# Kernel tuning notes

Measured on AMD Instinct MI355X. Metric: run time of the kernel, lower is better.

The kernel has to match this reference:

```python
import jax, jax.numpy as jnp
import numpy as np

C = 768
HEADS = 12
NF = 8      # num_frames
SL = 196    # seq_len (patches per frame)
B = 2
N = 1 + NF * SL
HID = 4 * C


def _ln(x, g, b, eps=1e-5):
    mu = jnp.mean(x, axis=-1, keepdims=True)
    var = jnp.mean((x - mu) ** 2, axis=-1, keepdims=True)
    return (x - mu) * jax.lax.rsqrt(var + eps) * g + b


def setup_inputs() -> dict:
    key = jax.random.key(0)
    ks = jax.random.split(key, 16)
    s = 0.02
    return {
        "x": jax.random.normal(ks[0], (B, N, C), jnp.float32),
        "g1": jnp.ones((C,), jnp.float32),
        "b1": jnp.zeros((C,), jnp.float32),
        "Wqkv": jax.random.normal(ks[1], (C, 3 * C), jnp.float32) * s,
        "Wq": jax.random.normal(ks[2], (C, C), jnp.float32) * s,
        "Wkv": jax.random.normal(ks[3], (C, 2 * C), jnp.float32) * s,
        "Wp": jax.random.normal(ks[4], (C, C), jnp.float32) * s,
        "bp": jnp.zeros((C,), jnp.float32),
        "g2": jnp.ones((C,), jnp.float32),
        "b2": jnp.zeros((C,), jnp.float32),
        "W1": jax.random.normal(ks[5], (C, HID), jnp.float32) * s,
        "bf1": jnp.zeros((HID,), jnp.float32),
        "W2": jax.random.normal(ks[6], (HID, C), jnp.float32) * s,
        "bf2": jnp.zeros((C,), jnp.float32),
        "seq_len": SL,
        "num_frames": NF,
    }


def _traj_attn(xn, Wqkv, Wq, Wkv, Wp, bp, P, F):
    Bb, Nn, Cc = xn.shape
    h = HEADS
    d = Cc // h
    scale = d ** -0.5
    S = F * P  # non-cls tokens

    qkv = xn @ Wqkv                                   # (B,N,3C)
    q, k, v = jnp.split(qkv, 3, axis=-1)

    def heads(t):  # (B,N,C) -> (B*h, N, d)
        return t.reshape(Bb, Nn, h, d).transpose(0, 2, 1, 3).reshape(Bb * h, Nn, d)

    q, k, v = heads(q), heads(k), heads(v)
    cls_q, q_ = q[:, :1], q[:, 1:]
    k_ = k[:, 1:]
    v_ = v[:, 1:]

    # cls token attends to all tokens
    sim = jnp.einsum('bid,bjd->bij', cls_q * scale, k)
    cls_out = jnp.einsum('bij,bjd->bid', jax.nn.softmax(sim, axis=-1), v)
    cls_out = cls_out.reshape(Bb, h, 1, d).transpose(0, 2, 1, 3).reshape(Bb, 1, Cc)

    # stage 1: space-only softmax per frame
    qk = jnp.einsum('bqd,bkd->bqk', q_, k_).reshape(Bb * h, S, F, P)
    space_attn = jax.nn.softmax(scale * qk, axis=-1)          # (Bh,S,F,P)
    v_r = v_.reshape(Bb * h, F, P, d)
    x1 = jnp.einsum('bqfn,bfnd->bqfd', space_attn, v_r)       # (Bh,S,F,d)
    x1 = x1.reshape(Bb, h, S, F, d).transpose(0, 2, 3, 1, 4).reshape(Bb, S, F, Cc)

    # diagonal across (query-frame, key-frame)
    xg = x1.reshape(Bb, F, P, F, Cc)
    diag = jnp.diagonal(xg, axis1=1, axis2=3)                 # (B,P,C,F)
    x_diag = diag.transpose(0, 3, 1, 2).reshape(Bb, S, Cc)    # b (f n) d

    # stage 2: frame-wise attention
    q2 = (x_diag @ Wq).reshape(Bb, S, h, d).transpose(0, 2, 1, 3) * scale  # bhsd
    kv2 = x1 @ Wkv
    k2, v2 = jnp.split(kv2, 2, axis=-1)
    k2 = k2.reshape(Bb, S, F, h, d).transpose(0, 3, 1, 2, 4)  # bhsfd
    attn2 = jax.nn.softmax(jnp.einsum('bhsd,bhsfd->bhsf', q2, k2), axis=-1)
    xo = x1.reshape(Bb, S, F, h, d).transpose(0, 3, 1, 2, 4)  # use_original_code=True
    out = jnp.einsum('bhsf,bhsfd->bhsd', attn2, xo)
    out = out.transpose(0, 2, 1, 3).reshape(Bb, S, Cc)

    out = jnp.concatenate([cls_out, out], axis=1) @ Wp + bp
    return out


def reference(x, g1, b1, Wqkv, Wq, Wkv, Wp, bp, g2, b2, W1, bf1, W2, bf2, seq_len, num_frames):
    x = x + _traj_attn(_ln(x, g1, b1), Wqkv, Wq, Wkv, Wp, bp, seq_len, num_frames)
    h = _ln(x, g2, b2)
    h = jax.nn.gelu(h @ W1 + bf1, approximate=False) @ W2 + bf2
    return x + h
```

## Files before the change

kernel.cpp:

```cpp
#include <hip/hip_runtime.h>
#include <hip/hip_bf16.h>
#include <math.h>

#define C     768
#define HEADS 12
#define HD    64
#define NF    8
#define SL    196
#define BB    2
#define NN    1569
#define SS    1568
#define HID   3072
#define CLS_CH 256
#define CLS_NC 7
#define QSCALE 0.18033688011112042f

typedef __attribute__((ext_vector_type(8))) short short8;
typedef __attribute__((ext_vector_type(4))) float f32x4;
typedef unsigned short u16;
typedef unsigned int u32;

__device__ inline float fast_exp2(float x) { return __builtin_amdgcn_exp2f(x); }

__device__ inline u16 f2b(float f) {
    __hip_bfloat16 h = __float2bfloat16(f);
    return *reinterpret_cast<u16*>(&h);
}
__device__ inline float b2f(u16 u) {
    union { unsigned u; float f; } v; v.u = ((unsigned)u) << 16;
    return v.f;
}

__device__ inline void gload_lds16(const void* g, void* l) {
    __builtin_amdgcn_global_load_lds(
        (const __attribute__((address_space(1))) void*)g,
        (__attribute__((address_space(3))) void*)l, 16, 0, 0);
}

__global__ void ln_kernel(const float* __restrict__ x, const float* __restrict__ g,
                          const float* __restrict__ b, u16* __restrict__ out, int rows) {
    int row = blockIdx.x;
    if (row >= rows) return;
    const float* xr = x + (size_t)row * C;
    int tid = threadIdx.x;
    float v[3];
    float sum = 0.f, sumsq = 0.f;
#pragma unroll
    for (int i = 0; i < 3; i++) {
        v[i] = xr[tid + 256 * i];
        sum += v[i]; sumsq += v[i] * v[i];
    }
    __shared__ float s1[4], s2[4];
    for (int off = 32; off; off >>= 1) {
        sum   += __shfl_xor(sum, off);
        sumsq += __shfl_xor(sumsq, off);
    }
    int wave = tid >> 6, lane = tid & 63;
    if (lane == 0) { s1[wave] = sum; s2[wave] = sumsq; }
    __syncthreads();
    sum   = s1[0] + s1[1] + s1[2] + s1[3];
    sumsq = s2[0] + s2[1] + s2[2] + s2[3];
    float mu  = sum / C;
    float var = sumsq / C - mu * mu;
    float rstd = rsqrtf(fmaxf(var, 0.f) + 1e-5f);
    u16* outr = out + (size_t)row * C;
#pragma unroll
    for (int i = 0; i < 3; i++) {
        int c = tid + 256 * i;
        outr[c] = f2b((v[i] - mu) * rstd * g[c] + b[c]);
    }
}

__global__ void wtrans_all_kernel(
    const float* __restrict__ Wqkv, const float* __restrict__ Wq,
    const float* __restrict__ Wkv,  const float* __restrict__ Wp,
    const float* __restrict__ W1,   const float* __restrict__ W2,
    u16* Tqkv, u16* Tq, u16* Tkv, u16* Tp, u16* T1, u16* T2) {
    __shared__ float tile[64][65];
    int bid = blockIdx.x;
    const float* W; u16* Wt; int K, ldb, gx;
    if (bid < 432)       { W = Wqkv; Wt = Tqkv; K = 768;  ldb = 2304; gx = 36; }
    else if (bid < 576)  { W = Wq;   Wt = Tq;   K = 768;  ldb = 768;  gx = 12; bid -= 432; }
    else if (bid < 720)  { W = Wkv;  Wt = Tkv;  K = 768;  ldb = 1536; gx = 12; bid -= 576; }
    else if (bid < 864)  { W = Wp;   Wt = Tp;   K = 768;  ldb = 768;  gx = 12; bid -= 720; }
    else if (bid < 1440) { W = W1;   Wt = T1;   K = 768;  ldb = 3072; gx = 48; bid -= 864; }
    else                 { W = W2;   Wt = T2;   K = 3072; ldb = 768;  gx = 12; bid -= 1440; }
    int nb = (bid % gx) * 64, kb = (bid / gx) * 64;
    int tx = threadIdx.x & 63, ty = threadIdx.x >> 6;
#pragma unroll
    for (int i = 0; i < 64; i += 4)
        tile[ty + i][tx] = W[(size_t)(kb + ty + i) * ldb + nb + tx];
    __syncthreads();
#pragma unroll
    for (int i = 0; i < 64; i += 4)
        Wt[(size_t)(nb + ty + i) * K + kb + tx] = f2b(tile[tx][ty + i]);
}

template<int MODE, int BM, int BN, int WAVES>
__global__ __launch_bounds__(WAVES * 64) void gemm_bf16(
    const u16* __restrict__ A, const u16* __restrict__ Bt,
    const float* __restrict__ bias, const float* resid, void* Cout,
    int M, int N, int K, int lda, int ldb, int gx) {
    constexpr int WCOLS = WAVES / 2;
    constexpr int WBN   = BN / WCOLS;
    constexpr int MT    = BM / 32;
    constexpr int NT    = WBN / 16;
    constexpr int ACH   = BM * 4;
    constexpr int TCH   = (BM + BN) * 4;
    constexpr int HALF  = (BM + BN) * 64;
    __shared__ char smem[2 * HALF];
    int tid = threadIdx.x, lane = tid & 63, wave = tid >> 6;
    int wr = wave / WCOLS, wc = wave % WCOLS;
    int r16 = lane & 15, kg = lane >> 4;

    int nwg = gridDim.x, orig = blockIdx.x;
    int qq = nwg >> 3, rr = nwg & 7, xcd = orig & 7, lid = orig >> 3;
    int wg = (xcd < rr ? xcd * (qq + 1) : rr * (qq + 1) + (xcd - rr) * qq) + lid;
    int bx = wg % gx, by = wg / gx;
    if constexpr (MODE == 4) {
        int mt_ = (M + BM - 1) / BM;
        int chunk = by / mt_; by -= chunk * mt_;
        A    += (size_t)chunk * K;
        Bt   += (size_t)chunk * K;
        Cout  = (void*)((float*)Cout + (size_t)chunk * ((size_t)M * N));
    }
    int row0 = by * BM, col0 = bx * BN;

    f32x4 acc[MT][NT];
#pragma unroll
    for (int mt = 0; mt < MT; mt++)
#pragma unroll
        for (int nt = 0; nt < NT; nt++) acc[mt][nt] = (f32x4){0.f, 0.f, 0.f, 0.f};

    auto stage = [&](char* dstbase, int ks) {
        int k0 = ks << 5;
#pragma unroll
        for (int it = 0; it < TCH / (WAVES * 64); it++) {
            int c = it * (WAVES * 64) + tid;
            const u16* src;
            if (c < ACH) {
                int ml = c >> 2, s = c & 3;
                int kgs = s ^ ((ml >> 1) & 3);
                int gm = row0 + ml; if (gm >= M) gm = M - 1;
                src = A + (size_t)gm * lda + k0 + kgs * 8;
            } else {
                int cc = c - ACH;
                int nl = cc >> 2, s = cc & 3;
                int kgs = s ^ ((nl >> 1) & 3);
                src = Bt + (size_t)(col0 + nl) * ldb + k0 + kgs * 8;
            }
            gload_lds16(src, dstbase + it * (WAVES * 1024) + wave * 1024);
        }
    };

    int nsteps = K >> 5;
    stage(smem, 0);
    __syncthreads();
    for (int ks = 0; ks < nsteps; ks++) {
        char* curb = smem + (ks & 1) * HALF;
        if (ks + 1 < nsteps) stage(smem + ((ks + 1) & 1) * HALF, ks + 1);
        short8 af[MT], bfr[NT];
#pragma unroll
        for (int mt = 0; mt < MT; mt++) {
            int ml = wr * (BM / 2) + mt * 16 + r16;
            af[mt] = *(const short8*)(curb + ml * 64 + ((kg ^ ((ml >> 1) & 3)) << 4));
        }
#pragma unroll
        for (int nt = 0; nt < NT; nt++) {
            int nl = wc * WBN + nt * 16 + r16;
            bfr[nt] = *(const short8*)(curb + BM * 64 + nl * 64 + ((kg ^ ((nl >> 1) & 3)) << 4));
        }
        __builtin_amdgcn_s_setprio(1);
#pragma unroll
        for (int mt = 0; mt < MT; mt++)
#pragma unroll
            for (int nt = 0; nt < NT; nt++)
                acc[mt][nt] = __builtin_amdgcn_mfma_f32_16x16x32_bf16(af[mt], bfr[nt], acc[mt][nt], 0, 0, 0);
        __builtin_amdgcn_s_setprio(0);
        __syncthreads();
    }
#pragma unroll
    for (int mt = 0; mt < MT; mt++) {
#pragma unroll
        for (int r2 = 0; r2 < 4; r2++) {
            int gm = row0 + wr * (BM / 2) + mt * 16 + kg * 4 + r2;
            if (gm >= M) continue;
#pragma unroll
            for (int nt = 0; nt < NT; nt++) {
                int gn = col0 + wc * WBN + nt * 16 + r16;
                float v = acc[mt][nt][r2];
                if constexpr (MODE == 1) {
                    v += bias[gn];
                    v = 0.5f * v * (1.f + erff(v * 0.70710678118f));
                }
                if constexpr (MODE == 2) {
                    v += bias[gn] + resid[(size_t)gm * N + gn];
                    ((float*)Cout)[(size_t)gm * N + gn] = v;
                } else if constexpr (MODE == 4) {
                    ((float*)Cout)[(size_t)gm * N + gn] = v;
                } else {
                    if constexpr (MODE == 3) { if (gn < 768) v *= QSCALE; }
                    ((u16*)Cout)[(size_t)gm * N + gn] = f2b(v);
                }
            }
        }
    }
}

__global__ void fc2_merge_kernel(const float* __restrict__ p,
                                 const float* __restrict__ bias, float* __restrict__ out) {
    int i = blockIdx.x * 256 + threadIdx.x;
    int total = BB * NN * (C / 4);
    if (i >= total) return;
    int c4 = i % (C / 4);
    size_t stride = (size_t)BB * NN * (C / 4);
    float4 bb = ((const float4*)bias)[c4];
    float4 a0 = ((const float4*)p)[i];
    float4 a1 = ((const float4*)p)[i + stride];
    float4 o  = ((float4*)out)[i];
    o.x += a0.x + a1.x + bb.x;
    o.y += a0.y + a1.y + bb.y;
    o.z += a0.z + a1.z + bb.z;
    o.w += a0.w + a1.w + bb.w;
    ((float4*)out)[i] = o;
}

__global__ void cls_partial_kernel(const u16* __restrict__ qkv, float* __restrict__ part) {
    int c = blockIdx.x, bh = blockIdx.y;
    int b = bh / HEADS, hh = bh % HEADS;
    int tid = threadIdx.x;
    int wave = tid >> 6, lane = tid & 63;
    __shared__ float s_q[HD];
    __shared__ float s_sc[CLS_CH];
    __shared__ float sm[4], ss[4];
    __shared__ float sacc[4][HD];
    if (tid < HD) s_q[tid] = b2f(qkv[(size_t)(b * NN) * 2304 + hh * HD + tid]);
    __syncthreads();

    int j0 = c * CLS_CH;
    int j = j0 + tid;
    float sc = -1e30f;
    if (j < NN) {
        const short8* kp = (const short8*)(qkv + ((size_t)(b * NN) + j) * 2304 + C + hh * HD);
        float acc = 0.f;
#pragma unroll
        for (int u = 0; u < 8; u++) {
            short8 kv = kp[u];
#pragma unroll
            for (int e = 0; e < 8; e++) acc += s_q[u * 8 + e] * b2f((u16)kv[e]);
        }
        sc = acc;
    }
    float m = sc;
    for (int off = 32; off; off >>= 1) m = fmaxf(m, __shfl_xor(m, off));
    if (lane == 0) sm[wave] = m;
    __syncthreads();
    m = fmaxf(fmaxf(sm[0], sm[1]), fmaxf(sm[2], sm[3]));
    float e = (j < NN) ? fast_exp2(sc - m) : 0.f;
    s_sc[tid] = e;
    float su = e;
    for (int off = 32; off; off >>= 1) su += __shfl_xor(su, off);
    if (lane == 0) ss[wave] = su;
    __syncthreads();
    float ssum = ss[0] + ss[1] + ss[2] + ss[3];

    int jj = tid >> 6, d = tid & 63;
    int jmax = NN - j0; if (jmax > CLS_CH) jmax = CLS_CH;
    const u16* vcol = qkv + ((size_t)(b * NN) + j0) * 2304 + 2 * C + hh * HD + d;
    float acc = 0.f;
    for (int t = jj; t < jmax; t += 4)
        acc += s_sc[t] * b2f(vcol[(size_t)t * 2304]);
    sacc[jj][d] = acc;
    __syncthreads();
    if (tid < HD) {
        float pv = sacc[0][tid] + sacc[1][tid] + sacc[2][tid] + sacc[3][tid];
        float* pp = part + ((size_t)bh * CLS_NC + c) * 66;
        pp[2 + tid] = pv;
        if (tid == 0) { pp[0] = m; pp[1] = ssum; }
    }
}

__global__ void cls_reduce_kernel(const float* __restrict__ part, u16* __restrict__ y) {
    int bh = blockIdx.x;
    int b = bh / HEADS, hh = bh % HEADS;
    int d = threadIdx.x;
    float gm = -1e30f;
#pragma unroll
    for (int c = 0; c < CLS_NC; c++)
        gm = fmaxf(gm, part[((size_t)bh * CLS_NC + c) * 66]);
    float tot = 0.f, pv = 0.f;
#pragma unroll
    for (int c = 0; c < CLS_NC; c++) {
        const float* pp = part + ((size_t)bh * CLS_NC + c) * 66;
        float w = fast_exp2(pp[0] - gm);
        tot += pp[1] * w;
        pv  += pp[2 + d] * w;
    }
    y[(size_t)(b * NN) * C + hh * HD + d] = f2b(pv / tot);
}

__global__ void repack_kv_kernel(const u16* __restrict__ qkv,
                                 u16* __restrict__ Kb, u16* __restrict__ Vt) {
    const int NK = 24 * NF * 208 * 8;
    const int NV = 24 * NF * 64 * 28;
    int t = blockIdx.x * 256 + threadIdx.x;
    if (t < NK) {
        int d8 = t & 7;
        int rest = t >> 3;
        int n = rest % 208;
        rest /= 208;
        int f = rest % NF;
        int bh = rest / NF;
        int b = bh / HEADS, h = bh % HEADS;
        short8 v = {0, 0, 0, 0, 0, 0, 0, 0};
        if (n < SL)
            v = *(const short8*)(qkv + ((size_t)(b * NN) + 1 + f * SL + n) * 2304 + C + h * HD + d8 * 8);
        *(short8*)(Kb + (((size_t)bh * NF + f) * 208 + n) * 64 + d8 * 8) = v;
    } else {
        int u = t - NK;
        if (u >= NV) return;
        int n8 = u % 28;
        int rest = u / 28;
        int d = rest % 64;
        rest /= 64;
        int f = rest % NF;
        int bh = rest / NF;
        int b = bh / HEADS, h = bh % HEADS;
        int n0 = n8 * 8;
        const u16* src = qkv + ((size_t)(b * NN) + 1 + f * SL) * 2304 + 2 * C + h * HD + d;
        short8 v;
#pragma unroll
        for (int jj = 0; jj < 8; jj++) {
            int n = n0 + jj;
            v[jj] = (n < SL) ? (short)src[(size_t)n * 2304] : (short)0;
        }
        *(short8*)(Vt + (((size_t)bh * NF + f) * 64 + d) * 224 + n0) = v;
    }
}

__global__ void space_attn_mfma(
    const u16* __restrict__ qkv, const u16* __restrict__ Kb,
    const u16* __restrict__ Vt, u16* __restrict__ x1, u16* __restrict__ xd) {
    __shared__ u16 smem[13312];
    int tid = threadIdx.x;
    int lane = tid & 63, wave = tid >> 6;
    int r16 = lane & 15, kg = lane >> 4;

    int n = blockIdx.x;
    int xcd = n & 7;
    int slot = n >> 3;
    int j = slot % 13;
    int gw = slot / 13;
    int bh = xcd * 3 + gw % 3;
    int f = gw / 3;
    int b = bh / HEADS, h = bh % HEADS;

    int sA = j * 8 + wave * 2, sB = sA + 1;
    bool actA = sA < 98, actB = sB < 98;
    int q0A = (actA ? sA : 97) * 16;
    int q0B = (actB ? sB : 97) * 16;

    const u16* qrowA = qkv + ((size_t)(b * NN) + 1 + q0A + r16) * 2304 + h * HD + kg * 8;
    const u16* qrowB = qkv + ((size_t)(b * NN) + 1 + q0B + r16) * 2304 + h * HD + kg * 8;
    short8 aqA0 = *(const short8*)(qrowA);
    short8 aqA1 = *(const short8*)(qrowA + 32);
    short8 aqB0 = *(const short8*)(qrowB);
    short8 aqB1 = *(const short8*)(qrowB + 32);

    const char* kb_g = (const char*)(Kb + ((size_t)bh * NF + f) * 208 * 64);
    for (int w = wave; w < 26; w += 4) {
        int p = w * 1024 + lane * 16;
        int row = p >> 7;
        int src = (p & ~127) | ((p & 127) ^ ((row & 7) << 4));
        gload_lds16(kb_g + src, (char*)smem + p);
    }
    __syncthreads();

    const char* ksm = (const char*)smem;
    int swz = (r16 & 7) << 4;
    bool tailz = (kg >= 1);
    const u16* vbase = Vt + ((size_t)bh * NF + f) * 64 * 224;

    f32x4 acc[13];
    u32 w0A[13], w1A[13], w0B[13], w1B[13];

#pragma unroll
    for (int t = 0; t < 13; t++) acc[t] = (f32x4){0.f, 0.f, 0.f, 0.f};
    __builtin_amdgcn_s_setprio(1);
#pragma unroll
    for (int t = 0; t < 13; t++) {
        const char* krow = ksm + (t * 16 + r16) * 128;
        short8 bk0 = *(const short8*)(krow + ((kg * 16) ^ swz));
        short8 bk1 = *(const short8*)(krow + ((64 + kg * 16) ^ swz));
        acc[t] = __builtin_amdgcn_mfma_f32_16x16x32_bf16(bk0, aqA0, acc[t], 0, 0, 0);
        acc[t] = __builtin_amdgcn_mfma_f32_16x16x32_bf16(bk1, aqA1, acc[t], 0, 0, 0);
    }
    __builtin_amdgcn_s_setprio(0);
    short8 vf[2][4];
#pragma unroll
    for (int dt = 0; dt < 4; dt++)
        vf[0][dt] = *(const short8*)(vbase + (dt * 16 + r16) * 224 + kg * 8);
    {
        float ssum = 0.f;
#pragma unroll
        for (int t = 0; t < 13; t++)
#pragma unroll
            for (int r = 0; r < 4; r++) {
                float p = (t == 12 && tailz) ? 0.f : fast_exp2(acc[t][r]);
                acc[t][r] = p;
                ssum += p;
            }
        ssum += __shfl_xor(ssum, 16);
        ssum += __shfl_xor(ssum, 32);
        float inv = 1.f / ssum;
#pragma unroll
        for (int t = 0; t < 13; t++) {
            w0A[t] = (u32)f2b(acc[t][0] * inv) | ((u32)f2b(acc[t][1] * inv) << 16);
            w1A[t] = (u32)f2b(acc[t][2] * inv) | ((u32)f2b(acc[t][3] * inv) << 16);
        }
    }

#pragma unroll
    for (int t = 0; t < 13; t++) acc[t] = (f32x4){0.f, 0.f, 0.f, 0.f};
    __builtin_amdgcn_s_setprio(1);
#pragma unroll
    for (int t = 0; t < 13; t++) {
        const char* krow = ksm + (t * 16 + r16) * 128;
        short8 bk0 = *(const short8*)(krow + ((kg * 16) ^ swz));
        short8 bk1 = *(const short8*)(krow + ((64 + kg * 16) ^ swz));
        acc[t] = __builtin_amdgcn_mfma_f32_16x16x32_bf16(bk0, aqB0, acc[t], 0, 0, 0);
        acc[t] = __builtin_amdgcn_mfma_f32_16x16x32_bf16(bk1, aqB1, acc[t], 0, 0, 0);
    }
    __builtin_amdgcn_s_setprio(0);
    {
        float ssum = 0.f;
#pragma unroll
        for (int t = 0; t < 13; t++)
#pragma unroll
            for (int r = 0; r < 4; r++) {
                float p = (t == 12 && tailz) ? 0.f : fast_exp2(acc[t][r]);
                acc[t][r] = p;
                ssum += p;
            }
        ssum += __shfl_xor(ssum, 16);
        ssum += __shfl_xor(ssum, 32);
        float inv = 1.f / ssum;
#pragma unroll
        for (int t = 0; t < 13; t++) {
            w0B[t] = (u32)f2b(acc[t][0] * inv) | ((u32)f2b(acc[t][1] * inv) << 16);
            w1B[t] = (u32)f2b(acc[t][2] * inv) | ((u32)f2b(acc[t][3] * inv) << 16);
        }
    }

    int src0 = r16 + ((kg & 1) << 5);
    int src1 = src0 + 16;
    bool thi = (kg >= 2);
    f32x4 oA[4], oB[4];
#pragma unroll
    for (int dt = 0; dt < 4; dt++) { oA[dt] = (f32x4){0.f, 0.f, 0.f, 0.f}; oB[dt] = (f32x4){0.f, 0.f, 0.f, 0.f}; }
    __builtin_amdgcn_s_setprio(1);
#pragma unroll
    for (int kc = 0; kc < 7; kc++) {
        if (kc < 6) {
#pragma unroll
            for (int dt = 0; dt < 4; dt++)
                vf[(kc + 1) & 1][dt] = *(const short8*)(vbase + (dt * 16 + r16) * 224 + (kc + 1) * 32 + kg * 8);
        }
        u32 a0, a1, b0, b1;
        if (kc == 6) {
            a0 = thi ? 0u : w0A[12]; a1 = thi ? 0u : w1A[12];
            b0 = thi ? 0u : w0B[12]; b1 = thi ? 0u : w1B[12];
        } else {
            a0 = thi ? w0A[2 * kc + 1] : w0A[2 * kc];
            a1 = thi ? w1A[2 * kc + 1] : w1A[2 * kc];
            b0 = thi ? w0B[2 * kc + 1] : w0B[2 * kc];
            b1 = thi ? w1B[2 * kc + 1] : w1B[2 * kc];
        }
        union { u32 u[4]; short8 s8; } pA, pB;
        pA.u[0] = (u32)__shfl((int)a0, src0);
        pA.u[1] = (u32)__shfl((int)a1, src0);
        pA.u[2] = (u32)__shfl((int)a0, src1);
        pA.u[3] = (u32)__shfl((int)a1, src1);
        pB.u[0] = (u32)__shfl((int)b0, src0);
        pB.u[1] = (u32)__shfl((int)b1, src0);
        pB.u[2] = (u32)__shfl((int)b0, src1);
        pB.u[3] = (u32)__shfl((int)b1, src1);
#pragma unroll
        for (int dt = 0; dt < 4; dt++) {
            oA[dt] = __builtin_amdgcn_mfma_f32_16x16x32_bf16(pA.s8, vf[kc & 1][dt], oA[dt], 0, 0, 0);
            oB[dt] = __builtin_amdgcn_mfma_f32_16x16x32_bf16(pB.s8, vf[kc & 1][dt], oB[dt], 0, 0, 0);
        }
    }
    __builtin_amdgcn_s_setprio(0);

    __syncthreads();
    u16* ebA = smem + wave * 2304;
    u16* ebB = ebA + 1152;
    int fbase = f * SL;
#pragma unroll
    for (int dt = 0; dt < 4; dt++)
#pragma unroll
        for (int r = 0; r < 4; r++) {
            ebA[(kg * 4 + r) * 72 + dt * 16 + r16] = f2b(oA[dt][r]);
            ebB[(kg * 4 + r) * 72 + dt * 16 + r16] = f2b(oB[dt][r]);
        }
    if (actA) {
        u16* x1row = x1 + (((size_t)(b * SS + q0A)) * NF + f) * C + h * HD;
        u16* xdrow = xd + ((size_t)(b * SS + q0A)) * C + h * HD;
#pragma unroll
        for (int it = 0; it < 2; it++) {
            int c = it * 64 + lane;
            int qr = c >> 3, c8 = c & 7;
            short8 v8 = *(const short8*)(&ebA[qr * 72 + c8 * 8]);
            *(short8*)(x1row + (size_t)qr * (NF * C) + c8 * 8) = v8;
            if ((unsigned)(q0A + qr - fbase) < (unsigned)SL)
                *(short8*)(xdrow + (size_t)qr * C + c8 * 8) = v8;
        }
    }
    if (actB) {
        u16* x1row = x1 + (((size_t)(b * SS + q0B)) * NF + f) * C + h * HD;
        u16* xdrow = xd + ((size_t)(b * SS + q0B)) * C + h * HD;
#pragma unroll
        for (int it = 0; it < 2; it++) {
            int c = it * 64 + lane;
            int qr = c >> 3, c8 = c & 7;
            short8 v8 = *(const short8*)(&ebB[qr * 72 + c8 * 8]);
            *(short8*)(x1row + (size_t)qr * (NF * C) + c8 * 8) = v8;
            if ((unsigned)(q0B + qr - fbase) < (unsigned)SL)
                *(short8*)(xdrow + (size_t)qr * C + c8 * 8) = v8;
        }
    }
}

__global__ void attn2_kernel(const u16* __restrict__ q2, const u16* __restrict__ k2,
                             const u16* __restrict__ x1, u16* __restrict__ y) {
    int item = blockIdx.x * 4 + (threadIdx.x >> 6);
    if (item >= BB * HEADS * SS) return;
    int lane = threadIdx.x & 63;
    int s = item % SS;
    int bh = item / SS;
    int b = bh / HEADS, hh = bh % HEADS;
    size_t rowbs = (size_t)(b * SS + s);
    float qv = b2f(q2[rowbs * C + hh * HD + lane]) * QSCALE;
    float lg[NF];
#pragma unroll
    for (int f = 0; f < NF; f++) {
        float p = qv * b2f(k2[(rowbs * NF + f) * C + hh * HD + lane]);
        for (int off = 32; off; off >>= 1) p += __shfl_xor(p, off);
        lg[f] = p;
    }
    float m = lg[0];
#pragma unroll
    for (int f = 1; f < NF; f++) m = fmaxf(m, lg[f]);
    float sum = 0.f;
#pragma unroll
    for (int f = 0; f < NF; f++) { lg[f] = fast_exp2(lg[f] - m); sum += lg[f]; }
    float inv = 1.f / sum;
    float acc = 0.f;
#pragma unroll
    for (int f = 0; f < NF; f++) acc += lg[f] * b2f(x1[(rowbs * NF + f) * C + hh * HD + lane]);
    y[((size_t)(b * NN) + 1 + s) * C + hh * HD + lane] = f2b(acc * inv);
}

extern "C" void kernel_launch(void* const* d_in, const int* in_sizes, int n_in,
                              void* d_out, int out_size, void* d_ws, size_t ws_size,
                              hipStream_t stream) {
    const float* x    = (const float*)d_in[0];
    const float* g1   = (const float*)d_in[1];
    const float* b1   = (const float*)d_in[2];
    const float* Wqkv = (const float*)d_in[3];
    const float* Wq   = (const float*)d_in[4];
    const float* Wkv  = (const float*)d_in[5];
    const float* Wp   = (const float*)d_in[6];
    const float* bp   = (const float*)d_in[7];
    const float* g2   = (const float*)d_in[8];
    const float* b2_  = (const float*)d_in[9];
    const float* W1   = (const float*)d_in[10];
    const float* bf1  = (const float*)d_in[11];
    const float* W2   = (const float*)d_in[12];
    const float* bf2  = (const float*)d_in[13];
    float* out = (float*)d_out;

    u16* us     = (u16*)d_ws;
    u16* xn_b   = us;
    u16* qkv_b  = xn_b   + 2409984;
    u16* Wt_qkv = qkv_b  + 7229952;
    u16* Wt_q   = Wt_qkv + 1769472;
    u16* Wt_kv  = Wt_q   + 589824;
    u16* Wt_p   = Wt_kv  + 589824;
    u16* W1t    = Wt_p   + 589824;
    u16* W2t    = W1t    + 2359296;
    u16* Kb     = W2t    + 2359296;
    u16* Vt     = Kb     + 2555904;
    u16* x1b    = Vt     + 2752512;
    u16* xdb    = x1b    + 19267584;
    u16* q2b    = xdb    + 2408448;
    u16* k2b    = q2b    + 2408448;
    u16* y_b    = k2b    + 19267584;
    u16* a1b    = y_b    + 2409984;
    float* cls_ws   = (float*)(a1b + 9639936);
    float* fc2_part = cls_ws + 24 * 7 * 66;

    const int M1 = BB * NN;
    const int M2 = BB * SS;
    const int M3 = BB * SS * NF;

    wtrans_all_kernel<<<2016, 256, 0, stream>>>(Wqkv, Wq, Wkv, Wp, W1, W2,
                                                Wt_qkv, Wt_q, Wt_kv, Wt_p, W1t, W2t);
    ln_kernel<<<M1, 256, 0, stream>>>(x, g1, b1, xn_b, M1);
    gemm_bf16<3, 128, 128, 8><<<18 * 25, 512, 0, stream>>>(
        xn_b, Wt_qkv, nullptr, nullptr, qkv_b, M1, 2304, 768, 768, 768, 18);
    repack_kv_kernel<<<(24 * NF * 208 * 8 + 24 * NF * 64 * 28 + 255) / 256, 256, 0, stream>>>(
        qkv_b, Kb, Vt);
    cls_partial_kernel<<<dim3(CLS_NC, BB * HEADS), 256, 0, stream>>>(qkv_b, cls_ws);
    cls_reduce_kernel<<<BB * HEADS, 64, 0, stream>>>(cls_ws, y_b);
    space_attn_mfma<<<2496, 256, 0, stream>>>(qkv_b, Kb, Vt, x1b, xdb);
    gemm_bf16<0, 64, 64, 4><<<12 * 49, 256, 0, stream>>>(
        xdb, Wt_q, nullptr, nullptr, q2b, M2, 768, 768, 768, 768, 12);
    gemm_bf16<0, 128, 128, 8><<<6 * 196, 512, 0, stream>>>(
        x1b, Wt_kv, nullptr, nullptr, k2b, M3, 768, 768, 768, 768, 6);
    attn2_kernel<<<(BB * HEADS * SS + 3) / 4, 256, 0, stream>>>(q2b, k2b, x1b, y_b);
    gemm_bf16<2, 64, 64, 4><<<12 * 50, 256, 0, stream>>>(
        y_b, Wt_p, bp, x, out, M1, 768, 768, 768, 768, 12);
    ln_kernel<<<M1, 256, 0, stream>>>(out, g2, b2_, xn_b, M1);
    gemm_bf16<1, 128, 128, 8><<<24 * 25, 512, 0, stream>>>(
        xn_b, W1t, bf1, nullptr, a1b, M1, 3072, 768, 768, 768, 24);
    gemm_bf16<4, 128, 64, 4><<<12 * 25 * 2, 256, 0, stream>>>(
        a1b, W2t, nullptr, nullptr, fc2_part, M1, 768, 1536, 3072, 3072, 12);
    fc2_merge_kernel<<<(BB * NN * (C / 4) + 255) / 256, 256, 0, stream>>>(
        fc2_part, bf2, out);
}
```

Baseline: 269.4 us.

## Fuse frame-wise attention into the K2 projection GEMM epilogue

Adds a GEMM epilogue mode that takes the K2 projection tile from registers, dots it with the corresponding q2 rows staged in shared memory, does the 8-way frame softmax, and combines x1 rows into the output. This removes the large k2 intermediate write and read and the separate attn2 kernel launch. The cost is extra shared-memory traffic, synchronisation, and uncoalesced x1 reloads inside the GEMM tail, and correctness depends on the tile mapping matching head and frame boundaries.

```diff
diff --git a/kernel.cpp b/kernel.cpp
--- a/kernel.cpp
+++ b/kernel.cpp
@@ -179,6 +179,71 @@
         __builtin_amdgcn_s_setprio(0);
         __syncthreads();
     }
+
+    if constexpr (MODE == 6) {
+        u16*   q2l = (u16*)smem;
+        float* sc2 = (float*)(smem + 4096);
+        float* Pl  = (float*)(smem + 6144);
+        const u16* q2p = (const u16*)resid;
+        {
+            int idx = tid * 4;
+            int sr = idx >> 7, cc = idx & 127;
+            *(uint2*)(q2l + idx) =
+                *(const uint2*)(q2p + (size_t)(by * 16 + sr) * 768 + bx * 128 + cc);
+        }
+        __syncthreads();
+#pragma unroll
+        for (int mt = 0; mt < MT; mt++) {
+#pragma unroll
+            for (int r2 = 0; r2 < 4; r2++) {
+                int row = wr * 64 + mt * 16 + kg * 4 + r2;
+                int sl = row >> 3;
+                float q0v = b2f(q2l[sl * 128 + wc * 32 + r16]);
+                float q1v = b2f(q2l[sl * 128 + wc * 32 + 16 + r16]);
+                float p = acc[mt][0][r2] * q0v + acc[mt][1][r2] * q1v;
+                p += __shfl_xor(p, 1); p += __shfl_xor(p, 2);
+                p += __shfl_xor(p, 4); p += __shfl_xor(p, 8);
+                if (r16 == 0)
+                    sc2[(row * 2 + (wc >> 1)) * 2 + (wc & 1)] = p;
+            }
+        }
+        __syncthreads();
+        if (tid < 32) {
+            int sl = tid >> 1, hl = tid & 1;
+            float sc[8];
+            float m = -1e30f;
+#pragma unroll
+            for (int ff = 0; ff < 8; ff++) {
+                int row = sl * 8 + ff;
+                sc[ff] = (sc2[(row * 2 + hl) * 2] + sc2[(row * 2 + hl) * 2 + 1]) * QSCALE;
+                m = fmaxf(m, sc[ff]);
+            }
+            float sum = 0.f;
+#pragma unroll
+            for (int ff = 0; ff < 8; ff++) { sc[ff] = fast_exp2(sc[ff] - m); sum += sc[ff]; }
+            float invp = 1.f / sum;
+#pragma unroll
+            for (int ff = 0; ff < 8; ff++) Pl[(sl * 2 + hl) * 8 + ff] = sc[ff] * invp;
+        }
+        __syncthreads();
+        u16* yp = (u16*)Cout;
+#pragma unroll
+        for (int pass = 0; pass < 4; pass++) {
+            int sl = pass * 4 + (tid >> 7);
+            int c  = tid & 127;
+            int hl = c >> 6;
+            int gs = by * 16 + sl;
+            float accv = 0.f;
+#pragma unroll
+            for (int ff = 0; ff < 8; ff++)
+                accv += Pl[(sl * 2 + hl) * 8 + ff] *
+                        b2f(A[(size_t)(gs * 8 + ff) * lda + bx * 128 + c]);
+            int bb = gs / SS, ss2 = gs % SS;
+            yp[((size_t)bb * NN + 1 + ss2) * C + bx * 128 + c] = f2b(accv);
+        }
+        return;
+    }
+
 #pragma unroll
     for (int mt = 0; mt < MT; mt++) {
 #pragma unroll
@@ -532,36 +597,6 @@
     }
 }
 
-__global__ void attn2_kernel(const u16* __restrict__ q2, const u16* __restrict__ k2,
-                             const u16* __restrict__ x1, u16* __restrict__ y) {
-    int item = blockIdx.x * 4 + (threadIdx.x >> 6);
-    if (item >= BB * HEADS * SS) return;
-    int lane = threadIdx.x & 63;
-    int s = item % SS;
-    int bh = item / SS;
-    int b = bh / HEADS, hh = bh % HEADS;
-    size_t rowbs = (size_t)(b * SS + s);
-    float qv = b2f(q2[rowbs * C + hh * HD + lane]) * QSCALE;
-    float lg[NF];
-#pragma unroll
-    for (int f = 0; f < NF; f++) {
-        float p = qv * b2f(k2[(rowbs * NF + f) * C + hh * HD + lane]);
-        for (int off = 32; off; off >>= 1) p += __shfl_xor(p, off);
-        lg[f] = p;
-    }
-    float m = lg[0];
-#pragma unroll
-    for (int f = 1; f < NF; f++) m = fmaxf(m, lg[f]);
-    float sum = 0.f;
-#pragma unroll
-    for (int f = 0; f < NF; f++) { lg[f] = fast_exp2(lg[f] - m); sum += lg[f]; }
-    float inv = 1.f / sum;
-    float acc = 0.f;
-#pragma unroll
-    for (int f = 0; f < NF; f++) acc += lg[f] * b2f(x1[(rowbs * NF + f) * C + hh * HD + lane]);
-    y[((size_t)(b * NN) + 1 + s) * C + hh * HD + lane] = f2b(acc * inv);
-}
-
 extern "C" void kernel_launch(void* const* d_in, const int* in_sizes, int n_in,
                               void* d_out, int out_size, void* d_ws, size_t ws_size,
                               hipStream_t stream) {
@@ -595,8 +630,7 @@
     u16* x1b    = Vt     + 2752512;
     u16* xdb    = x1b    + 19267584;
     u16* q2b    = xdb    + 2408448;
-    u16* k2b    = q2b    + 2408448;
-    u16* y_b    = k2b    + 19267584;
+    u16* y_b    = q2b    + 2408448;
     u16* a1b    = y_b    + 2409984;
     float* cls_ws   = (float*)(a1b + 9639936);
     float* fc2_part = cls_ws + 24 * 7 * 66;
@@ -617,9 +651,8 @@
     space_attn_mfma<<<2496, 256, 0, stream>>>(qkv_b, Kb, Vt, x1b, xdb);
     gemm_bf16<0, 64, 64, 4><<<12 * 49, 256, 0, stream>>>(
         xdb, Wt_q, nullptr, nullptr, q2b, M2, 768, 768, 768, 768, 12);
-    gemm_bf16<0, 128, 128, 8><<<6 * 196, 512, 0, stream>>>(
-        x1b, Wt_kv, nullptr, nullptr, k2b, M3, 768, 768, 768, 768, 6);
-    attn2_kernel<<<(BB * HEADS * SS + 3) / 4, 256, 0, stream>>>(q2b, k2b, x1b, y_b);
+    gemm_bf16<6, 128, 128, 8><<<6 * 196, 512, 0, stream>>>(
+        x1b, Wt_kv, nullptr, (const float*)q2b, y_b, M3, 768, 768, 768, 768, 6);
     gemm_bf16<2, 64, 64, 4><<<12 * 50, 256, 0, stream>>>(
         y_b, Wt_p, bp, x, out, M1, 768, 768, 768, 768, 12);
     ln_kernel<<<M1, 256, 0, stream>>>(out, g2, b2_, xn_b, M1);
```

Result: faster. 254.1 us (-5.7%).
